# Kernel tuning notes

Measured on AMD Instinct MI355X. Metric: run time of the kernel, lower is better.

The kernel has to match this reference:

```python
import jax, jax.numpy as jnp
import numpy as np
import math

HIDDEN = 512
BATCH, SEQ = 4, 4096


def setup_inputs() -> dict:
    key = jax.random.key(0)
    ks = jax.random.split(key, 7)
    s = 1.0 / math.sqrt(HIDDEN)
    return {
        "X": jax.random.normal(ks[0], (BATCH, SEQ, HIDDEN), dtype=jnp.float32),
        "Wq": jax.random.uniform(ks[1], (HIDDEN, HIDDEN), jnp.float32, -s, s),
        "bq": jax.random.uniform(ks[2], (HIDDEN,), jnp.float32, -s, s),
        "Wk": jax.random.uniform(ks[3], (HIDDEN, HIDDEN), jnp.float32, -s, s),
        "bk": jax.random.uniform(ks[4], (HIDDEN,), jnp.float32, -s, s),
        "Wv": jax.random.uniform(ks[5], (HIDDEN, HIDDEN), jnp.float32, -s, s),
        "bv": jax.random.uniform(ks[6], (HIDDEN,), jnp.float32, -s, s),
    }


def reference(X, Wq, bq, Wk, bk, Wv, bv):
    # Q, K, V projections (torch Linear: y = x @ W.T + b; here W stored as [in, out])
    Q = jnp.einsum("bsd,de->bse", X, Wq) + bq
    K = jnp.einsum("bsd,de->bse", X, Wk) + bk
    V = jnp.einsum("bsd,de->bse", X, Wv) + bv
    scale = 1.0 / math.sqrt(Q.shape[-1])
    scores = jnp.einsum("bqd,bkd->bqk", Q, K) * scale  # [B, S, S]
    weights = jax.nn.softmax(scores, axis=-1)
    return jnp.einsum("bqk,bkd->bqd", weights, V)
```

## Files before the change

kernel.cpp:

```cpp
#include <hip/hip_runtime.h>
#include <hip/hip_bf16.h>
#include <math.h>


typedef __bf16 bfx8 __attribute__((ext_vector_type(8)));
typedef __bf16 bfx4 __attribute__((ext_vector_type(4)));
typedef float  fx4  __attribute__((ext_vector_type(4)));

#define HID   512
#define NBATCH 4
#define SEQ   4096
#define MROWS (NBATCH * SEQ)

#if __has_builtin(__builtin_amdgcn_exp2f)
#define EXPFN(x) __builtin_amdgcn_exp2f(x)
#define QSCALE 0.06375871589f
#else
#define EXPFN(x) __expf(x)
#define QSCALE 0.04419417382f
#endif

constexpr int MODE_QKV = 0;
constexpr int MODE_EXP = 2;
constexpr int MODE_DIV = 3;

__device__ __forceinline__ void gload_lds16(const __bf16* gsrc, __bf16* ldst) {
  __builtin_amdgcn_global_load_lds(
      (const __attribute__((address_space(1))) unsigned int*)gsrc,
      (__attribute__((address_space(3))) unsigned int*)ldst,
      16, 0, 0);
}

__global__ void prep_x_kernel(const float* __restrict__ X, __bf16* __restrict__ Xb) {
  int i = (blockIdx.x * 256 + threadIdx.x) * 4;
  const float4 v = *(const float4*)(X + i);
  bfx4 o;
  o[0] = (__bf16)v.x; o[1] = (__bf16)v.y; o[2] = (__bf16)v.z; o[3] = (__bf16)v.w;
  *(bfx4*)(Xb + i) = o;
}

__global__ void prep_w_kernel(const float* __restrict__ Wq, const float* __restrict__ Wk,
                              const float* __restrict__ Wv, __bf16* __restrict__ Wt) {
  int id  = blockIdx.x * 256 + threadIdx.x;
  int g   = id >> 18;
  int rem = id & ((1 << 18) - 1);
  int i   = rem >> 9;
  int o   = rem & 511;
  const float* W = (g == 0) ? Wq : ((g == 1) ? Wk : Wv);
  Wt[(g << 18) + (o << 9) + i] = (__bf16)W[rem];
}

template <int MODE, int TM, int TN>
__global__ __launch_bounds__(256)
void gemm_bt(const __bf16* __restrict__ A, const __bf16* __restrict__ B,
             void* __restrict__ C0v, void* __restrict__ C1v, void* __restrict__ C2v,
             const float* __restrict__ b0, const float* __restrict__ b1,
             const float* __restrict__ b2, float* __restrict__ rowsum,
             int lda, int ldb, int ldc, int K_,
             long sA, long sB, long sC, int sR) {
  constexpr int MT = TM / 32;
  constexpr int NT = TN / 32;
  constexpr int ABE = (TM + TN) * 64;
  constexpr int CTE = (MODE == MODE_DIV) ? TM * TN * 2 : TM * TN;
  constexpr int LDSN = (ABE > CTE) ? ABE : CTE;
  __shared__ __bf16 L[LDSN];
  __bf16* As = L;
  __bf16* Bs = L + TM * 64;

  const int z = blockIdx.z;
  A += (long)z * sA;
  B += (long)z * sB;

  const int tid  = threadIdx.x;
  const int lane = tid & 63;
  const int w    = tid >> 6;
  const int wm   = w >> 1, wn = w & 1;
  const int lm   = lane & 15, lq = lane >> 4;

  const int row0 = blockIdx.y * TM;
  const int col0 = blockIdx.x * TN;

  const __bf16* Ag = A + (long)row0 * lda;
  const __bf16* Bg = B + (long)col0 * ldb;

  fx4 acc[MT][NT] = {};

  for (int kt = 0; kt < K_; kt += 64) {
    __syncthreads();
#pragma unroll
    for (int it = 0; it < TM / 32; ++it) {
      int s = it * 256 + tid;
      int r = s >> 3, c = ((s & 7) ^ (r & 7)) << 3;
      gload_lds16(Ag + (long)r * lda + kt + c, As + it * 2048 + w * 512);
    }
#pragma unroll
    for (int it = 0; it < TN / 32; ++it) {
      int s = it * 256 + tid;
      int r = s >> 3, c = ((s & 7) ^ (r & 7)) << 3;
      gload_lds16(Bg + (long)r * ldb + kt + c, Bs + it * 2048 + w * 512);
    }
    __syncthreads();
#pragma unroll
    for (int kk = 0; kk < 2; ++kk) {
      bfx8 af[MT], bfr[NT];
#pragma unroll
      for (int t = 0; t < MT; ++t) {
        int ra = wm * (TM / 2) + t * 16 + lm;
        af[t] = *(const bfx8*)(As + ra * 64 + (((kk * 4 + lq) ^ (ra & 7)) << 3));
      }
#pragma unroll
      for (int t = 0; t < NT; ++t) {
        int rb = wn * (TN / 2) + t * 16 + lm;
        bfr[t] = *(const bfx8*)(Bs + rb * 64 + (((kk * 4 + lq) ^ (rb & 7)) << 3));
      }
#pragma unroll
      for (int mt = 0; mt < MT; ++mt)
#pragma unroll
        for (int nt = 0; nt < NT; ++nt)
          acc[mt][nt] = __builtin_amdgcn_mfma_f32_16x16x32_bf16(af[mt], bfr[nt],
                                                                acc[mt][nt], 0, 0, 0);
    }
  }

  const int lr0 = wm * (TM / 2);
  const int lc0 = wn * (TN / 2);

  __syncthreads();

  if constexpr (MODE == MODE_QKV) {
    const int g   = col0 >> 9;
    const int gc  = col0 & 511;
    const float* bias = (g == 0) ? b0 : ((g == 1) ? b1 : b2);
    float bvv[NT];
#pragma unroll
    for (int nt = 0; nt < NT; ++nt) bvv[nt] = bias[gc + lc0 + nt * 16 + lm];

    if (g < 2) {
      __bf16* Ct = L;
#pragma unroll
      for (int mt = 0; mt < MT; ++mt)
#pragma unroll
        for (int nt = 0; nt < NT; ++nt)
#pragma unroll
          for (int i = 0; i < 4; ++i) {
            float v = acc[mt][nt][i] + bvv[nt];
            if (g == 0) v *= QSCALE;
            Ct[(lr0 + mt * 16 + lq * 4 + i) * TN + lc0 + nt * 16 + lm] = (__bf16)v;
          }
      __syncthreads();
      __bf16* C = (g == 0) ? (__bf16*)C0v : (__bf16*)C1v;
#pragma unroll
      for (int j = 0; j < TM * TN / 2048; ++j) {
        int s = j * 256 + tid;
        int off = s * 8;
        int r = off / TN, c = off % TN;
        *(bfx8*)(C + (long)(row0 + r) * ldc + gc + c) = *(const bfx8*)(Ct + off);
      }
    } else {
      __bf16* C = (__bf16*)C2v;
#pragma unroll
      for (int mt = 0; mt < MT; ++mt)
#pragma unroll
        for (int nt = 0; nt < NT; ++nt) {
          int c  = gc + lc0 + nt * 16 + lm;
          int rb = row0 + lr0 + mt * 16 + lq * 4;
          int b  = rb >> 12;
          int s  = rb & 4095;
          bfx4 pk;
#pragma unroll
          for (int i = 0; i < 4; ++i) pk[i] = (__bf16)(acc[mt][nt][i] + bvv[nt]);
          *(bfx4*)(C + ((long)b * HID + c) * SEQ + s) = pk;
        }
    }
  } else if constexpr (MODE == MODE_EXP) {
    __bf16* Ct = L;
    float* rsump = rowsum + (long)z * sR;
#pragma unroll
    for (int mt = 0; mt < MT; ++mt)
#pragma unroll
      for (int i = 0; i < 4; ++i) {
        int rl = lr0 + mt * 16 + lq * 4 + i;
        float rs = 0.f;
#pragma unroll
        for (int nt = 0; nt < NT; ++nt) {
          float e = EXPFN(acc[mt][nt][i]);
          Ct[rl * TN + lc0 + nt * 16 + lm] = (__bf16)e;
          rs += e;
        }
        rs += __shfl_xor(rs, 1);
        rs += __shfl_xor(rs, 2);
        rs += __shfl_xor(rs, 4);
        rs += __shfl_xor(rs, 8);
        if (lm == 0) atomicAdd(&rsump[row0 + rl], rs);
      }
    __syncthreads();
    __bf16* C = ((__bf16*)C0v) + (long)z * sC;
#pragma unroll
    for (int j = 0; j < TM * TN / 2048; ++j) {
      int s = j * 256 + tid;
      int off = s * 8;
      int r = off / TN, c = off % TN;
      *(bfx8*)(C + (long)(row0 + r) * ldc + col0 + c) = *(const bfx8*)(Ct + off);
    }
  } else {
    float* Cf = (float*)L;
    const float* rsump = rowsum + (long)z * sR;
#pragma unroll
    for (int mt = 0; mt < MT; ++mt)
#pragma unroll
      for (int i = 0; i < 4; ++i) {
        int rl = lr0 + mt * 16 + lq * 4 + i;
        float inv = 1.f / rsump[row0 + rl];
#pragma unroll
        for (int nt = 0; nt < NT; ++nt)
          Cf[rl * TN + lc0 + nt * 16 + lm] = acc[mt][nt][i] * inv;
      }
    __syncthreads();
    float* C = ((float*)C0v) + (long)z * sC;
#pragma unroll
    for (int j = 0; j < TM * TN / 1024; ++j) {
      int s = j * 256 + tid;
      int off = s * 4;
      int r = off / TN, c = off % TN;
      *(float4*)(C + (long)(row0 + r) * ldc + col0 + c) = *(const float4*)(Cf + off);
    }
  }
}

extern "C" void kernel_launch(void* const* d_in, const int* in_sizes, int n_in,
                              void* d_out, int out_size, void* d_ws, size_t ws_size,
                              hipStream_t stream) {
  (void)in_sizes; (void)n_in; (void)out_size; (void)ws_size;
  const float* X  = (const float*)d_in[0];
  const float* Wq = (const float*)d_in[1];
  const float* bq = (const float*)d_in[2];
  const float* Wk = (const float*)d_in[3];
  const float* bk = (const float*)d_in[4];
  const float* Wv = (const float*)d_in[5];
  const float* bv = (const float*)d_in[6];
  float* out = (float*)d_out;

  __bf16* Xb     = (__bf16*)d_ws;
  __bf16* Wt     = Xb + (long)MROWS * HID;
  __bf16* Q      = Wt + 3 * HID * HID;
  __bf16* Kb     = Q + (long)MROWS * HID;
  __bf16* Vt     = Kb + (long)MROWS * HID;
  float*  rowsum = (float*)(Vt + (long)MROWS * HID);
  __bf16* E      = (__bf16*)(rowsum + MROWS);

  prep_x_kernel<<<(MROWS * HID) / 1024, 256, 0, stream>>>(X, Xb);
  prep_w_kernel<<<(3 * HID * HID) / 256, 256, 0, stream>>>(Wq, Wk, Wv, Wt);

  (void)hipMemsetAsync(rowsum, 0, MROWS * sizeof(float), stream);

  gemm_bt<MODE_QKV, 128, 128><<<dim3(12, 128, 1), 256, 0, stream>>>(
      Xb, Wt, Q, Kb, Vt, bq, bk, bv, nullptr,
      HID, HID, HID, HID, 0, 0, 0, 0);

  gemm_bt<MODE_EXP, 128, 128><<<dim3(32, 32, NBATCH), 256, 0, stream>>>(
      Q, Kb, E, nullptr, nullptr, nullptr, nullptr, nullptr, rowsum,
      HID, HID, SEQ, HID, (long)SEQ * HID, (long)SEQ * HID, (long)SEQ * SEQ, SEQ);

  gemm_bt<MODE_DIV, 64, 128><<<dim3(4, 64, NBATCH), 256, 0, stream>>>(
      E, Vt, out, nullptr, nullptr, nullptr, nullptr, nullptr, rowsum,
      SEQ, SEQ, HID, SEQ, (long)SEQ * SEQ, (long)HID * SEQ, (long)SEQ * HID, SEQ);
}
```

Measured before the change: 338.3 us.

## Fuse QK^T, exp and PV into a single flash-attention kernel

Replaces the two-GEMM path, which wrote the full exponentiated score matrix to global memory and read it back, with a fused kernel. Each block holds a 64-row Q tile in LDS, streams K and V tiles from global with register double-buffering, writes exp'd scores into a swizzled LDS P tile, and accumulates the PV product and row sums in registers. This removes the large intermediate score-matrix traffic and the rowsum memset, at the cost of one block per CU and heavy register/LDS use. Like the previous code, the softmax is computed without subtracting the row maximum.

```diff
diff --git a/kernel.cpp b/kernel.cpp
--- a/kernel.cpp
+++ b/kernel.cpp
@@ -227,6 +227,156 @@
   }
 }
 
+#define QK_STEP(CUR, NXT, DS, LOAD)                                          \
+    {                                                                        \
+      _Pragma("unroll")                                                      \
+      for (int nt = 0; nt < 4; ++nt)                                         \
+        if (LOAD) NXT[nt] = *(const bfx8*)(kp + (long)nt * (16 * HID) +      \
+                                           ((DS) + 1) * 32);                 \
+      __builtin_amdgcn_s_setprio(1);                                         \
+      _Pragma("unroll")                                                      \
+      for (int mt = 0; mt < 4; ++mt) {                                       \
+        const int r = mt * 16 + lm;                                          \
+        bfx8 af = *(const bfx8*)(Qs + r * 512 + (((DS) >> 1) << 6) +         \
+                   ((((((DS) & 1) << 2) + lq) ^ (r & 7)) << 3));             \
+        _Pragma("unroll")                                                    \
+        for (int nt = 0; nt < 4; ++nt)                                       \
+          s4[mt][nt] = __builtin_amdgcn_mfma_f32_16x16x32_bf16(af, CUR[nt],  \
+                         s4[mt][nt], 0, 0, 0);                               \
+      }                                                                      \
+      __builtin_amdgcn_s_setprio(0);                                         \
+    }
+
+#define PV_STEP(CUR, NXT, KS, LOAD)                                          \
+    {                                                                        \
+      _Pragma("unroll")                                                      \
+      for (int nt = 0; nt < 4; ++nt)                                         \
+        if (LOAD) NXT[nt] = *(const bfx8*)(vp + (long)nt * (16 * SEQ) +      \
+                                           ((KS) + 1) * 32);                 \
+      __builtin_amdgcn_s_setprio(1);                                         \
+      _Pragma("unroll")                                                      \
+      for (int mt = 0; mt < 4; ++mt) {                                       \
+        const int r = mt * 16 + lm;                                          \
+        bfx8 pa = *(const bfx8*)(Ps + r * 512 +                              \
+                   ((((KS) * 4 + lq) ^ (r & 7)) << 3));                      \
+        _Pragma("unroll")                                                    \
+        for (int nt = 0; nt < 4; ++nt)                                       \
+          o[mt][nt] = __builtin_amdgcn_mfma_f32_16x16x32_bf16(pa, CUR[nt],   \
+                        o[mt][nt], 0, 0, 0);                                 \
+      }                                                                      \
+      __builtin_amdgcn_s_setprio(0);                                         \
+    }
+
+__global__ __launch_bounds__(512, 2)
+void flash_attn(const __bf16* __restrict__ Qg_, const __bf16* __restrict__ Kg_,
+                const __bf16* __restrict__ Vg_, float* __restrict__ Og_) {
+  __shared__ __bf16 Qs[64 * 512];
+  __shared__ __bf16 Ps[64 * 512];
+  __shared__ float  rsw[8 * 64];
+
+  const int tid  = threadIdx.x;
+  const int lane = tid & 63;
+  const int w    = tid >> 6;
+  const int lm   = lane & 15;
+  const int lq   = lane >> 4;
+
+  const int bid = blockIdx.x;
+  const int z   = (bid & 7) >> 1;
+  const int qb  = ((bid & 1) << 5) | (bid >> 3);
+  const long q0 = (long)qb * 64;
+
+  const __bf16* Qg = Qg_ + ((long)z * SEQ + q0) * HID;
+  const __bf16* Kg = Kg_ + (long)z * SEQ * HID;
+  const __bf16* Vg = Vg_ + (long)z * HID * SEQ;
+  float*        Og = Og_ + ((long)z * SEQ + q0) * HID;
+
+#pragma unroll
+  for (int it = 0; it < 8; ++it) {
+    int idx = it * 512 + tid;
+    int r   = idx >> 6;
+    int c6  = idx & 63;
+    int src = (c6 & ~7) | ((c6 ^ r) & 7);
+    gload_lds16(Qg + (long)r * HID + src * 8, Qs + (it * 512 + w * 64) * 8);
+  }
+
+  fx4 o[4][4]  = {};
+  fx4 rs4[4]   = {};
+
+  const __bf16* kp = Kg + (long)(w * 64 + lm) * HID + lq * 8;
+  const __bf16* vp = Vg + (long)(w * 64 + lm) * SEQ + lq * 8;
+
+  __syncthreads();
+
+  for (int kt = 0; kt < 8; ++kt) {
+    fx4 s4[4][4] = {};
+    bfx8 bkA[4], bkB[4];
+#pragma unroll
+    for (int nt = 0; nt < 4; ++nt)
+      bkA[nt] = *(const bfx8*)(kp + (long)nt * (16 * HID));
+#pragma unroll
+    for (int g = 0; g < 8; ++g) {
+      QK_STEP(bkA, bkB, 2 * g, 1)
+      QK_STEP(bkB, bkA, 2 * g + 1, (g < 7))
+    }
+    kp += (long)512 * HID;
+
+    __syncthreads();
+
+#pragma unroll
+    for (int mt = 0; mt < 4; ++mt)
+#pragma unroll
+      for (int i = 0; i < 4; ++i) {
+        const int r = mt * 16 + lq * 4 + i;
+#pragma unroll
+        for (int nt = 0; nt < 4; ++nt) {
+          float e = EXPFN(s4[mt][nt][i]);
+          rs4[mt][i] += e;
+          const int c = w * 64 + nt * 16 + lm;
+          Ps[r * 512 + ((((c >> 3) ^ (r & 7)) << 3) | (c & 7))] = (__bf16)e;
+        }
+      }
+    __syncthreads();
+
+    bfx8 bvA[4], bvB[4];
+#pragma unroll
+    for (int nt = 0; nt < 4; ++nt)
+      bvA[nt] = *(const bfx8*)(vp + (long)nt * (16 * SEQ));
+#pragma unroll
+    for (int g = 0; g < 8; ++g) {
+      PV_STEP(bvA, bvB, 2 * g, 1)
+      PV_STEP(bvB, bvA, 2 * g + 1, (g < 7))
+    }
+    vp += 512;
+  }
+
+#pragma unroll
+  for (int mt = 0; mt < 4; ++mt)
+#pragma unroll
+    for (int i = 0; i < 4; ++i) {
+      float v = rs4[mt][i];
+      v += __shfl_xor(v, 1);
+      v += __shfl_xor(v, 2);
+      v += __shfl_xor(v, 4);
+      v += __shfl_xor(v, 8);
+      if (lm == 0) rsw[w * 64 + mt * 16 + lq * 4 + i] = v;
+    }
+  __syncthreads();
+
+#pragma unroll
+  for (int mt = 0; mt < 4; ++mt)
+#pragma unroll
+    for (int i = 0; i < 4; ++i) {
+      const int r = mt * 16 + lq * 4 + i;
+      float t = rsw[r];
+#pragma unroll
+      for (int ww = 1; ww < 8; ++ww) t += rsw[ww * 64 + r];
+      const float inv = 1.f / t;
+#pragma unroll
+      for (int nt = 0; nt < 4; ++nt)
+        Og[(long)r * HID + w * 64 + nt * 16 + lm] = o[mt][nt][i] * inv;
+    }
+}
+
 extern "C" void kernel_launch(void* const* d_in, const int* in_sizes, int n_in,
                               void* d_out, int out_size, void* d_ws, size_t ws_size,
                               hipStream_t stream) {
@@ -240,28 +390,18 @@
   const float* bv = (const float*)d_in[6];
   float* out = (float*)d_out;
 
-  __bf16* Xb     = (__bf16*)d_ws;
-  __bf16* Wt     = Xb + (long)MROWS * HID;
-  __bf16* Q      = Wt + 3 * HID * HID;
-  __bf16* Kb     = Q + (long)MROWS * HID;
-  __bf16* Vt     = Kb + (long)MROWS * HID;
-  float*  rowsum = (float*)(Vt + (long)MROWS * HID);
-  __bf16* E      = (__bf16*)(rowsum + MROWS);
+  __bf16* Xb = (__bf16*)d_ws;
+  __bf16* Wt = Xb + (long)MROWS * HID;
+  __bf16* Q  = Wt + 3 * HID * HID;
+  __bf16* Kb = Q + (long)MROWS * HID;
+  __bf16* Vt = Kb + (long)MROWS * HID;
 
   prep_x_kernel<<<(MROWS * HID) / 1024, 256, 0, stream>>>(X, Xb);
   prep_w_kernel<<<(3 * HID * HID) / 256, 256, 0, stream>>>(Wq, Wk, Wv, Wt);
-
-  (void)hipMemsetAsync(rowsum, 0, MROWS * sizeof(float), stream);
 
   gemm_bt<MODE_QKV, 128, 128><<<dim3(12, 128, 1), 256, 0, stream>>>(
       Xb, Wt, Q, Kb, Vt, bq, bk, bv, nullptr,
       HID, HID, HID, HID, 0, 0, 0, 0);
 
-  gemm_bt<MODE_EXP, 128, 128><<<dim3(32, 32, NBATCH), 256, 0, stream>>>(
-      Q, Kb, E, nullptr, nullptr, nullptr, nullptr, nullptr, rowsum,
-      HID, HID, SEQ, HID, (long)SEQ * HID, (long)SEQ * HID, (long)SEQ * SEQ, SEQ);
-
-  gemm_bt<MODE_DIV, 64, 128><<<dim3(4, 64, NBATCH), 256, 0, stream>>>(
-      E, Vt, out, nullptr, nullptr, nullptr, nullptr, nullptr, rowsum,
-      SEQ, SEQ, HID, SEQ, (long)SEQ * SEQ, (long)HID * SEQ, (long)SEQ * HID, SEQ);
-}
+  flash_attn<<<dim3(256), 512, 0, stream>>>(Q, Kb, Vt, out);
+}
```

Measured after the change: 397.2 us. 17.4% more time.
